# Performance work log

Measured on AMD Instinct MI355X. Metric: run time of the kernel, lower is better.

## Reference

```python
import jax, jax.numpy as jnp
import numpy as np

H = 256  # hidden_size
T = 4096  # sequence length
IN = 128  # input_size


def _lstm_dir(x_seq, Wih, Whh, b, reverse):
    # x_seq: [T, D_in]; Wih: [4H, D_in]; Whh: [4H, H]; b: [4H]
    xs = x_seq @ Wih.T + b  # precompute input projection [T, 4H]
    if reverse:
        xs = xs[::-1]

    def step(carry, xt):
        h, c = carry
        z = xt + h @ Whh.T
        i, f, g, o = jnp.split(z, 4, axis=-1)  # torch gate order i,f,g,o
        c = jax.nn.sigmoid(f) * c + jax.nn.sigmoid(i) * jnp.tanh(g)
        h = jax.nn.sigmoid(o) * jnp.tanh(c)
        return (h, c), h

    init = (jnp.zeros((H,), x_seq.dtype), jnp.zeros((H,), x_seq.dtype))
    _, hs = jax.lax.scan(step, init, xs)
    if reverse:
        hs = hs[::-1]
    return hs  # [T, H]


def _bilstm_layer(x_seq, Wih_f, Whh_f, b_f, Wih_b, Whh_b, b_b):
    hf = _lstm_dir(x_seq, Wih_f, Whh_f, b_f, False)
    hb = _lstm_dir(x_seq, Wih_b, Whh_b, b_b, True)
    return jnp.concatenate([hf, hb], axis=-1)  # [T, 2H]


def setup_inputs() -> dict:
    key = jax.random.key(0)
    ks = jax.random.split(key, 20)
    s = 1.0 / np.sqrt(H)

    def g(k, shape):
        return (jax.random.normal(k, shape, dtype=jnp.float32) * s)

    inp = {
        "x": jax.random.normal(ks[0], (1, T, IN), dtype=jnp.float32),
        # layer 0 (input dim IN), fwd / bwd directions; b = b_ih + b_hh folded
        "wih_l0f": g(ks[1], (4 * H, IN)), "whh_l0f": g(ks[2], (4 * H, H)), "b_l0f": g(ks[3], (4 * H,)),
        "wih_l0b": g(ks[4], (4 * H, IN)), "whh_l0b": g(ks[5], (4 * H, H)), "b_l0b": g(ks[6], (4 * H,)),
        # layer 1 (input dim 2H)
        "wih_l1f": g(ks[7], (4 * H, 2 * H)), "whh_l1f": g(ks[8], (4 * H, H)), "b_l1f": g(ks[9], (4 * H,)),
        "wih_l1b": g(ks[10], (4 * H, 2 * H)), "whh_l1b": g(ks[11], (4 * H, H)), "b_l1b": g(ks[12], (4 * H,)),
        # fc1: Linear(512, 256); fc2: Linear(256, 256)
        "fc1_w": g(ks[13], (256, 512)), "fc1_b": g(ks[14], (256,)),
        "fc2_w": g(ks[15], (256, 256)), "fc2_b": g(ks[16], (256,)),
    }
    return inp


def reference(x, wih_l0f, whh_l0f, b_l0f, wih_l0b, whh_l0b, b_l0b,
              wih_l1f, whh_l1f, b_l1f, wih_l1b, whh_l1b, b_l1b,
              fc1_w, fc1_b, fc2_w, fc2_b):
    xs = x[0]  # squeeze batch of 1 -> [T, IN]
    h1 = _bilstm_layer(xs, wih_l0f, whh_l0f, b_l0f, wih_l0b, whh_l0b, b_l0b)  # [T, 512]
    h2 = _bilstm_layer(h1, wih_l1f, whh_l1f, b_l1f, wih_l1b, whh_l1b, b_l1b)  # [T, 512]
    z = jnp.maximum(h2 @ fc1_w.T + fc1_b, 0.0)  # ReLU(fc1)
    e = z @ fc2_w.T + fc2_b  # [T, 256]
    # fused pairwise cosine similarity (replaces the per-row python loop)
    norms = jnp.linalg.norm(e, axis=1)  # [T]
    cs = (e @ e.T) / (norms[:, None] * norms[None, :])
    cs = jnp.maximum(cs, 1e-6)  # torch.clamp(min=1e-6)
    return 1.0 - cs  # [T, T]
```

## Files before the change

kernel.cpp:

```cpp
#include <hip/hip_runtime.h>
#include <hip/hip_fp16.h>

#define T_LEN 4096
#define HID   256
#define G4    1024

typedef unsigned int u32;
typedef _Float16 half2_t __attribute__((ext_vector_type(2)));

__device__ __forceinline__ float dot2f(u32 w, u32 h, float acc) {
#if __has_builtin(__builtin_amdgcn_fdot2)
    return __builtin_amdgcn_fdot2(__builtin_bit_cast(half2_t, w),
                                  __builtin_bit_cast(half2_t, h), acc, false);
#else
    __half2 wh = __builtin_bit_cast(__half2, w);
    __half2 hh = __builtin_bit_cast(__half2, h);
    float2 wf = __half22float2(wh), hf = __half22float2(hh);
    return acc + wf.x * hf.x + wf.y * hf.y;
#endif
}

__device__ __forceinline__ u32 pack2(float a, float b) {
    unsigned short lo = __half_as_ushort(__float2half(a));
    unsigned short hi = __half_as_ushort(__float2half(b));
    return ((u32)hi << 16) | (u32)lo;
}

__global__ void k_transpose(const float* __restrict__ in, float* __restrict__ out,
                            int N, int K) {
    int q = blockIdx.x * 256 + threadIdx.x;
    if (q >= N * K) return;
    int n = q / K, k = q % K;
    out[(size_t)k * N + n] = in[q];
}

__global__ void k_pack_whh(const float* __restrict__ W,
                           u32* __restrict__ rp, u32* __restrict__ lp) {
    int q = blockIdx.x * 256 + threadIdx.x;
    if (q < 512 * 192) {
        int tid = q / 192, j = q % 192;
        int row = (j < 96) ? tid : tid + 512;
        int p = j % 96;
        rp[q] = pack2(W[row * 256 + 2 * p], W[row * 256 + 2 * p + 1]);
    } else {
        int qq = q - 512 * 192;
        if (qq < 1024 * 32) {
            int row = qq / 32, j = qq % 32;
            lp[qq] = pack2(W[row * 256 + 192 + 2 * j], W[row * 256 + 192 + 2 * j + 1]);
        }
    }
}

__global__ __launch_bounds__(256) void k_gemm(
    const float* __restrict__ A, const float* __restrict__ Wt,
    const float* __restrict__ bias, const float* __restrict__ norms,
    float* __restrict__ C, int M, int N, int K, int mode) {
    __shared__ float As[16 * 512];
    const int tid = threadIdx.x;
    const int m0 = blockIdx.x * 16;
    const int n  = blockIdx.y * 256 + tid;

    for (int i = tid; i < 16 * K; i += 256) As[i] = A[(size_t)m0 * K + i];
    __syncthreads();

    float acc[16];
#pragma unroll
    for (int m = 0; m < 16; ++m) acc[m] = 0.f;

#pragma unroll 4
    for (int k = 0; k < K; ++k) {
        float w = Wt[(size_t)k * N + n];
#pragma unroll
        for (int m = 0; m < 16; ++m) acc[m] += As[m * K + k] * w;
    }

    float bn = bias ? bias[n] : 0.f;
#pragma unroll
    for (int m = 0; m < 16; ++m) {
        float v = acc[m] + bn;
        if (mode == 1) v = fmaxf(v, 0.f);
        if (mode == 2) {
            float d = norms[m0 + m] * norms[n];
            v = 1.f - fmaxf(acc[m] / d, 1e-6f);
        }
        C[(size_t)(m0 + m) * N + n] = v;
    }
}

__global__ void k_norms(const float* __restrict__ e, float* __restrict__ norms) {
    int i = blockIdx.x, lane = threadIdx.x;
    float s = 0.f;
    for (int k = lane; k < 256; k += 64) { float v = e[i * 256 + k]; s += v * v; }
    for (int off = 32; off; off >>= 1) s += __shfl_down(s, off);
    if (lane == 0) norms[i] = sqrtf(s);
}

__global__ __launch_bounds__(512, 2) void k_scan(
    const float* __restrict__ xs, const u32* __restrict__ rp,
    const u32* __restrict__ lp, float* __restrict__ hout) {
    __shared__ alignas(16) u32 wl[1024 * 34];
    __shared__ alignas(16) u32 hlds[128];
    __shared__ float zsh[512];

    const int tid = threadIdx.x;
    const int dir = blockIdx.x;
    xs += (size_t)dir * (T_LEN * G4);
    rp += (size_t)dir * (512 * 192);
    lp += (size_t)dir * (1024 * 32);

    for (int i = tid; i < 1024 * 32; i += 512) {
        int row = i >> 5, j = i & 31;
        wl[row * 34 + j] = lp[i];
    }
    if (tid < 128) hlds[tid] = 0u;

    u32 regw[192];
    {
        const uint4* rp4 = (const uint4*)(rp + (size_t)tid * 192);
#pragma unroll
        for (int p = 0; p < 48; ++p) {
            uint4 v = rp4[p];
            regw[4 * p + 0] = v.x; regw[4 * p + 1] = v.y;
            regw[4 * p + 2] = v.z; regw[4 * p + 3] = v.w;
        }
    }
    const int r0 = tid, r1 = tid + 512;
    float cst = 0.f;
    __syncthreads();

    int tt = dir ? (T_LEN - 1) : 0;
    float xn0 = xs[(size_t)tt * G4 + r0];
    float xn1 = xs[(size_t)tt * G4 + r1];

    for (int t = 0; t < T_LEN; ++t) {
        float a0 = xn0, a1 = xn1;
        int tn = dir ? ((t + 1 < T_LEN) ? T_LEN - 2 - t : 0)
                     : ((t + 1 < T_LEN) ? t + 1 : T_LEN - 1);
        xn0 = xs[(size_t)tn * G4 + r0];
        xn1 = xs[(size_t)tn * G4 + r1];

#pragma unroll
        for (int c = 0; c < 3; ++c) {
            u32 hh[32];
#pragma unroll
            for (int q = 0; q < 8; ++q) {
                uint4 v = *(const uint4*)&hlds[c * 32 + 4 * q];
                hh[4 * q + 0] = v.x; hh[4 * q + 1] = v.y;
                hh[4 * q + 2] = v.z; hh[4 * q + 3] = v.w;
            }
#pragma unroll
            for (int p = 0; p < 32; ++p) {
                a0 = dot2f(regw[c * 32 + p],      hh[p], a0);
                a1 = dot2f(regw[96 + c * 32 + p], hh[p], a1);
            }
        }
#pragma unroll
        for (int s = 0; s < 4; ++s) {
            u32 hh[8], w0[8], w1[8];
            uint4 hv0 = *(const uint4*)&hlds[96 + 8 * s];
            uint4 hv1 = *(const uint4*)&hlds[96 + 8 * s + 4];
            hh[0] = hv0.x; hh[1] = hv0.y; hh[2] = hv0.z; hh[3] = hv0.w;
            hh[4] = hv1.x; hh[5] = hv1.y; hh[6] = hv1.z; hh[7] = hv1.w;
#pragma unroll
            for (int u = 0; u < 4; ++u) {
                uint2 wa = *(const uint2*)&wl[r0 * 34 + 8 * s + 2 * u];
                w0[2 * u] = wa.x; w0[2 * u + 1] = wa.y;
                uint2 wb = *(const uint2*)&wl[r1 * 34 + 8 * s + 2 * u];
                w1[2 * u] = wb.x; w1[2 * u + 1] = wb.y;
            }
#pragma unroll
            for (int p = 0; p < 8; ++p) {
                a0 = dot2f(w0[p], hh[p], a0);
                a1 = dot2f(w1[p], hh[p], a1);
            }
        }

        if (tid >= 256) { zsh[tid - 256] = a0; zsh[256 + (tid - 256)] = a1; }
        __syncthreads();
        if (tid < 256) {
            float zi = a0, zg = a1;
            float zf = zsh[tid], zo = zsh[256 + tid];
            float si = 1.f / (1.f + __expf(-zi));
            float sf = 1.f / (1.f + __expf(-zf));
            float so = 1.f / (1.f + __expf(-zo));
            float tg = 1.f - 2.f / (__expf(2.f * zg) + 1.f);
            cst = sf * cst + si * tg;
            float th = 1.f - 2.f / (__expf(2.f * cst) + 1.f);
            float hv = so * th;
            hout[(size_t)tt * 512 + dir * 256 + tid] = hv;
            ((__half*)hlds)[tid] = __float2half(hv);
        }
        __syncthreads();
        tt = tn;
    }
}

extern "C" void kernel_launch(void* const* d_in, const int* in_sizes, int n_in,
                              void* d_out, int out_size, void* d_ws, size_t ws_size,
                              hipStream_t stream) {
    const float* x       = (const float*)d_in[0];
    const float* wih_l0f = (const float*)d_in[1];
    const float* whh_l0f = (const float*)d_in[2];
    const float* b_l0f   = (const float*)d_in[3];
    const float* wih_l0b = (const float*)d_in[4];
    const float* whh_l0b = (const float*)d_in[5];
    const float* b_l0b   = (const float*)d_in[6];
    const float* wih_l1f = (const float*)d_in[7];
    const float* whh_l1f = (const float*)d_in[8];
    const float* b_l1f   = (const float*)d_in[9];
    const float* wih_l1b = (const float*)d_in[10];
    const float* whh_l1b = (const float*)d_in[11];
    const float* b_l1b   = (const float*)d_in[12];
    const float* fc1_w   = (const float*)d_in[13];
    const float* fc1_b   = (const float*)d_in[14];
    const float* fc2_w   = (const float*)d_in[15];
    const float* fc2_b   = (const float*)d_in[16];
    float* outp = (float*)d_out;

    char* ws = (char*)d_ws;
    size_t off = 0;
    auto alloc = [&](size_t nbytes) {
        char* p = ws + off;
        off += (nbytes + 255) & ~(size_t)255;
        return p;
    };
    float* xs0   = (float*)alloc((size_t)2 * T_LEN * G4 * 4);
    float* xs1   = (float*)alloc((size_t)2 * T_LEN * G4 * 4);
    float* h1    = (float*)alloc((size_t)T_LEN * 512 * 4);
    float* h2    = (float*)alloc((size_t)T_LEN * 512 * 4);
    float* zb    = (float*)alloc((size_t)T_LEN * 256 * 4);
    float* eb    = (float*)alloc((size_t)T_LEN * 256 * 4);
    float* etb   = (float*)alloc((size_t)T_LEN * 256 * 4);
    float* nrm   = (float*)alloc((size_t)T_LEN * 4);
    float* wt0f  = (float*)alloc((size_t)128 * 1024 * 4);
    float* wt0b  = (float*)alloc((size_t)128 * 1024 * 4);
    float* wt1f  = (float*)alloc((size_t)512 * 1024 * 4);
    float* wt1b  = (float*)alloc((size_t)512 * 1024 * 4);
    float* wtf1  = (float*)alloc((size_t)512 * 256 * 4);
    float* wtf2  = (float*)alloc((size_t)256 * 256 * 4);
    u32*   rp0   = (u32*)alloc((size_t)2 * 512 * 192 * 4);
    u32*   lp0   = (u32*)alloc((size_t)2 * 1024 * 32 * 4);
    u32*   rp1   = (u32*)alloc((size_t)2 * 512 * 192 * 4);
    u32*   lp1   = (u32*)alloc((size_t)2 * 1024 * 32 * 4);

    k_transpose<<<(1024 * 128 + 255) / 256, 256, 0, stream>>>(wih_l0f, wt0f, 1024, 128);
    k_transpose<<<(1024 * 128 + 255) / 256, 256, 0, stream>>>(wih_l0b, wt0b, 1024, 128);
    k_transpose<<<(1024 * 512 + 255) / 256, 256, 0, stream>>>(wih_l1f, wt1f, 1024, 512);
    k_transpose<<<(1024 * 512 + 255) / 256, 256, 0, stream>>>(wih_l1b, wt1b, 1024, 512);
    k_transpose<<<(256 * 512 + 255) / 256, 256, 0, stream>>>(fc1_w, wtf1, 256, 512);
    k_transpose<<<(256 * 256 + 255) / 256, 256, 0, stream>>>(fc2_w, wtf2, 256, 256);

    const int packN = (512 * 192 + 1024 * 32 + 255) / 256;
    k_pack_whh<<<packN, 256, 0, stream>>>(whh_l0f, rp0,                lp0);
    k_pack_whh<<<packN, 256, 0, stream>>>(whh_l0b, rp0 + 512 * 192,    lp0 + 1024 * 32);
    k_pack_whh<<<packN, 256, 0, stream>>>(whh_l1f, rp1,                lp1);
    k_pack_whh<<<packN, 256, 0, stream>>>(whh_l1b, rp1 + 512 * 192,    lp1 + 1024 * 32);

    dim3 g1024(T_LEN / 16, 4);
    k_gemm<<<g1024, 256, 0, stream>>>(x, wt0f, b_l0f, nullptr, xs0, T_LEN, 1024, 128, 0);
    k_gemm<<<g1024, 256, 0, stream>>>(x, wt0b, b_l0b, nullptr, xs0 + (size_t)T_LEN * G4, T_LEN, 1024, 128, 0);
    k_scan<<<2, 512, 0, stream>>>(xs0, rp0, lp0, h1);
    k_gemm<<<g1024, 256, 0, stream>>>(h1, wt1f, b_l1f, nullptr, xs1, T_LEN, 1024, 512, 0);
    k_gemm<<<g1024, 256, 0, stream>>>(h1, wt1b, b_l1b, nullptr, xs1 + (size_t)T_LEN * G4, T_LEN, 1024, 512, 0);
    k_scan<<<2, 512, 0, stream>>>(xs1, rp1, lp1, h2);
    k_gemm<<<dim3(T_LEN / 16, 1), 256, 0, stream>>>(h2, wtf1, fc1_b, nullptr, zb, T_LEN, 256, 512, 1);
    k_gemm<<<dim3(T_LEN / 16, 1), 256, 0, stream>>>(zb, wtf2, fc2_b, nullptr, eb, T_LEN, 256, 256, 0);
    k_transpose<<<(T_LEN * 256 + 255) / 256, 256, 0, stream>>>(eb, etb, T_LEN, 256);
    k_norms<<<T_LEN, 64, 0, stream>>>(eb, nrm);
    k_gemm<<<dim3(T_LEN / 16, T_LEN / 256), 256, 0, stream>>>(eb, etb, nullptr, nrm, outp, T_LEN, T_LEN, 256, 2);
}
```

Before: 14.77 ms.

## Transpose LDS weight layout, split gate activations across thread halves

Repacks the LDS-resident slice of the recurrent weights into a k-major interleaved layout. Each thread now reads consecutive uint2 entries across the wavefront without the padded row stride, and the LDS array drops from 34 to 32 words per row. The upper thread half now computes the forget and output sigmoids before the barrier, so the lower half only evaluates the input and cell gate activations on the serial path. It also removes the two-blocks-per-CU launch bound hint and reorganises the register-weight dot products into smaller h chunks, which changes register pressure and LDS load scheduling.

Measured after the change: 19.17 ms. 1.3x slower.

```diff
diff --git a/kernel.cpp b/kernel.cpp
--- a/kernel.cpp
+++ b/kernel.cpp
@@ -46,7 +46,8 @@
         int qq = q - 512 * 192;
         if (qq < 1024 * 32) {
             int row = qq / 32, j = qq % 32;
-            lp[qq] = pack2(W[row * 256 + 192 + 2 * j], W[row * 256 + 192 + 2 * j + 1]);
+            int dst = (j >> 1) * 2048 + row * 2 + (j & 1);
+            lp[dst] = pack2(W[row * 256 + 192 + 2 * j], W[row * 256 + 192 + 2 * j + 1]);
         }
     }
 }
@@ -95,10 +96,10 @@
     if (lane == 0) norms[i] = sqrtf(s);
 }
 
-__global__ __launch_bounds__(512, 2) void k_scan(
+__global__ __launch_bounds__(512) void k_scan(
     const float* __restrict__ xs, const u32* __restrict__ rp,
     const u32* __restrict__ lp, float* __restrict__ hout) {
-    __shared__ alignas(16) u32 wl[1024 * 34];
+    __shared__ alignas(16) u32 wl[1024 * 32];
     __shared__ alignas(16) u32 hlds[128];
     __shared__ float zsh[512];
 
@@ -108,10 +109,7 @@
     rp += (size_t)dir * (512 * 192);
     lp += (size_t)dir * (1024 * 32);
 
-    for (int i = tid; i < 1024 * 32; i += 512) {
-        int row = i >> 5, j = i & 31;
-        wl[row * 34 + j] = lp[i];
-    }
+    for (int i = tid; i < 1024 * 32; i += 512) wl[i] = lp[i];
     if (tid < 128) hlds[tid] = 0u;
 
     u32 regw[192];
@@ -125,6 +123,7 @@
         }
     }
     const int r0 = tid, r1 = tid + 512;
+    const uint2* wl2 = (const uint2*)wl;
     float cst = 0.f;
     __syncthreads();
 
@@ -140,50 +139,47 @@
         xn1 = xs[(size_t)tn * G4 + r1];
 
 #pragma unroll
-        for (int c = 0; c < 3; ++c) {
-            u32 hh[32];
+        for (int c = 0; c < 12; ++c) {
+            uint4 h0 = *(const uint4*)&hlds[8 * c];
+            uint4 h1 = *(const uint4*)&hlds[8 * c + 4];
+            u32 hh[8] = {h0.x, h0.y, h0.z, h0.w, h1.x, h1.y, h1.z, h1.w};
 #pragma unroll
             for (int q = 0; q < 8; ++q) {
-                uint4 v = *(const uint4*)&hlds[c * 32 + 4 * q];
-                hh[4 * q + 0] = v.x; hh[4 * q + 1] = v.y;
-                hh[4 * q + 2] = v.z; hh[4 * q + 3] = v.w;
+                a0 = dot2f(regw[8 * c + q],      hh[q], a0);
+                a1 = dot2f(regw[96 + 8 * c + q], hh[q], a1);
             }
-#pragma unroll
-            for (int p = 0; p < 32; ++p) {
-                a0 = dot2f(regw[c * 32 + p],      hh[p], a0);
-                a1 = dot2f(regw[96 + c * 32 + p], hh[p], a1);
+        }
+#pragma unroll
+        for (int s = 0; s < 4; ++s) {
+            uint4 h0 = *(const uint4*)&hlds[96 + 8 * s];
+            uint4 h1 = *(const uint4*)&hlds[96 + 8 * s + 4];
+            u32 hh[8] = {h0.x, h0.y, h0.z, h0.w, h1.x, h1.y, h1.z, h1.w};
+            uint2 A[4], B[4];
+#pragma unroll
+            for (int l = 0; l < 4; ++l) {
+                A[l] = wl2[(4 * s + l) * 1024 + r0];
+                B[l] = wl2[(4 * s + l) * 1024 + r1];
             }
-        }
-#pragma unroll
-        for (int s = 0; s < 4; ++s) {
-            u32 hh[8], w0[8], w1[8];
-            uint4 hv0 = *(const uint4*)&hlds[96 + 8 * s];
-            uint4 hv1 = *(const uint4*)&hlds[96 + 8 * s + 4];
-            hh[0] = hv0.x; hh[1] = hv0.y; hh[2] = hv0.z; hh[3] = hv0.w;
-            hh[4] = hv1.x; hh[5] = hv1.y; hh[6] = hv1.z; hh[7] = hv1.w;
-#pragma unroll
-            for (int u = 0; u < 4; ++u) {
-                uint2 wa = *(const uint2*)&wl[r0 * 34 + 8 * s + 2 * u];
-                w0[2 * u] = wa.x; w0[2 * u + 1] = wa.y;
-                uint2 wb = *(const uint2*)&wl[r1 * 34 + 8 * s + 2 * u];
-                w1[2 * u] = wb.x; w1[2 * u + 1] = wb.y;
+#pragma unroll
+            for (int l = 0; l < 4; ++l) {
+                a0 = dot2f(A[l].x, hh[2 * l],     a0);
+                a0 = dot2f(A[l].y, hh[2 * l + 1], a0);
+                a1 = dot2f(B[l].x, hh[2 * l],     a1);
+                a1 = dot2f(B[l].y, hh[2 * l + 1], a1);
             }
-#pragma unroll
-            for (int p = 0; p < 8; ++p) {
-                a0 = dot2f(w0[p], hh[p], a0);
-                a1 = dot2f(w1[p], hh[p], a1);
-            }
-        }
-
-        if (tid >= 256) { zsh[tid - 256] = a0; zsh[256 + (tid - 256)] = a1; }
+        }
+
+        if (tid >= 256) {
+            float sf = 1.f / (1.f + __expf(-a0));
+            float so = 1.f / (1.f + __expf(-a1));
+            zsh[tid - 256] = sf;
+            zsh[tid]       = so;
+        }
         __syncthreads();
         if (tid < 256) {
-            float zi = a0, zg = a1;
-            float zf = zsh[tid], zo = zsh[256 + tid];
-            float si = 1.f / (1.f + __expf(-zi));
-            float sf = 1.f / (1.f + __expf(-zf));
-            float so = 1.f / (1.f + __expf(-zo));
-            float tg = 1.f - 2.f / (__expf(2.f * zg) + 1.f);
+            float si = 1.f / (1.f + __expf(-a0));
+            float tg = 1.f - 2.f / (__expf(2.f * a1) + 1.f);
+            float sf = zsh[tid], so = zsh[256 + tid];
             cst = sf * cst + si * tg;
             float th = 1.f - 2.f / (__expf(2.f * cst) + 1.f);
             float hv = so * th;
```
